# Kernel tuning notes

Hardware: AMD Instinct MI355X
Metric: run time of the kernel (lower is better)

## Reference

```python
import jax, jax.numpy as jnp
import numpy as np

B, L, C = 16, 450, 768
MID = 256
K = 8912
TEMP = 0.07
ENT_TEMP = 0.01
EPS_NORM = 1e-12


def _l2norm(v):
    n = jnp.sqrt(jnp.sum(v * v, axis=-1, keepdims=True))
    return v / jnp.maximum(n, EPS_NORM)


def setup_inputs() -> dict:
    key = jax.random.key(0)
    k1, k2, k3, k4 = jax.random.split(key, 4)
    x = jax.random.normal(k1, (B, L, C), dtype=jnp.float32)
    W_down = jax.random.normal(k2, (C, MID), dtype=jnp.float32) * (1.0 / np.sqrt(C))
    b_down = jnp.zeros((MID,), dtype=jnp.float32)
    bound = 1.0 / np.sqrt(MID)
    embedding = jax.random.uniform(k3, (K, MID), dtype=jnp.float32, minval=-bound, maxval=bound)
    return {"x": x, "W_down": W_down, "b_down": b_down, "embedding": embedding}


def reference(x, W_down, b_down, embedding):
    Bx, Lx, Cx = x.shape
    # down projection: [B,L,C] -> [B,L,MID]
    z = jnp.einsum('blc,cm->blm', x, W_down) + b_down
    zf = z.reshape(Bx * Lx, MID)
    zn = _l2norm(zf)                       # [N, MID]
    en = _l2norm(embedding)                # [K, MID]
    # squared euclidean distance on the unit sphere: ||a-b||^2 = 2 - 2 a.b
    d = 2.0 - 2.0 * jnp.einsum('nm,km->nk', zn, en)   # [N, K]
    idx = jnp.argmin(d, axis=1)            # [N]
    # codebook usage (no-grad stats)
    occ = jnp.bincount(idx, length=K)
    code_book_usage = jnp.mean((occ > 0).astype(jnp.float32))
    # soft assignment probs (hard_quant branch)
    logits = -d / TEMP
    probs = jax.nn.softmax(logits, axis=1)
    z_q = en[idx]                          # [N, MID]
    vq_loss = jnp.mean((z_q - jax.lax.stop_gradient(zn)) ** 2)
    commit_loss = jnp.mean((jax.lax.stop_gradient(z_q) - zn) ** 2)
    # straight-through estimator
    z_q_ste = zn + jax.lax.stop_gradient(z_q - zn)
    # entropy loss on affinity = -d at entropy temperature
    fa = -d / ENT_TEMP
    p = jax.nn.softmax(fa, axis=-1)
    lp = jax.nn.log_softmax(fa, axis=-1)
    avg_probs = jnp.mean(p, axis=0)
    avg_entropy = -jnp.sum(avg_probs * jnp.log(avg_probs + 1e-5))
    sample_entropy = -jnp.mean(jnp.sum(p * lp, axis=-1))
    entropy_loss = sample_entropy - avg_entropy
    return (z_q_ste.reshape(Bx, Lx, MID), probs.reshape(Bx, Lx, K),
            code_book_usage, vq_loss, commit_loss, entropy_loss)
```

## Files before the change

kernel.cpp:

```cpp
#include <hip/hip_runtime.h>
#include <stdint.h>

#define N_TOK 7200
#define N_PAD 7232
#define K_CODE 8912
#define K_PAD 8960
#define N_KT 140
#define MID 256
#define C_DIM 768
#define INV_TEMP (1.0f/0.07f)
#define INV_ETEMP 100.0f
#define MARGIN 0.02f
#define CAND_CAP 64
#define EPS_N 1e-12f

typedef __attribute__((ext_vector_type(8))) short short8;
typedef __attribute__((ext_vector_type(4))) float f32x4;

__device__ __forceinline__ unsigned short f2bf(float f) {
    unsigned u = __float_as_uint(f);
    u += 0x7fffu + ((u >> 16) & 1u);
    return (unsigned short)(u >> 16);
}
__device__ __forceinline__ float bf2f(unsigned short h) {
    return __uint_as_float(((unsigned)h) << 16);
}
__device__ __forceinline__ void nt_store4(float* p, float a, float b, float c, float d) {
    f32x4 v; v.x = a; v.y = b; v.z = c; v.w = d;
    __builtin_nontemporal_store(v, (f32x4*)p);
}

__global__ void k_prep(const float* __restrict__ emb,
                       float* __restrict__ en, unsigned short* __restrict__ en_h,
                       const float* __restrict__ W,
                       unsigned short* __restrict__ wt_h, unsigned short* __restrict__ wt_l,
                       const float* __restrict__ x,
                       unsigned short* __restrict__ xh_g, unsigned short* __restrict__ xl_g,
                       float* __restrict__ ap_acc, int* __restrict__ used,
                       float* __restrict__ acc4, int* __restrict__ ccnt) {
    __shared__ float sb[256];
    int b = blockIdx.x, t = threadIdx.x;
    if (b < K_CODE) {
        float v = emb[b * MID + t];
        sb[t] = v * v; __syncthreads();
        for (int s = 128; s > 0; s >>= 1) { if (t < s) sb[t] += sb[t + s]; __syncthreads(); }
        float nn = sqrtf(sb[0]);
        float o = v / fmaxf(nn, EPS_N);
        en[b * MID + t] = o;
        en_h[b * MID + t] = f2bf(o);
    } else if (b < K_CODE + 768) {
        int i = (b - K_CODE) * 256 + t;
        int c = i / MID, tc = i % MID;
        float v = W[i];
        unsigned short h = f2bf(v);
        unsigned short l = f2bf(v - bf2f(h));
        wt_h[tc * C_DIM + c] = h;
        wt_l[tc * C_DIM + c] = l;
    } else if (b < K_CODE + 768 + 5400) {
        size_t i4 = ((size_t)(b - K_CODE - 768) * 256 + t) * 4;
        float4 v = *(const float4*)(x + i4);
        unsigned short h0 = f2bf(v.x), h1 = f2bf(v.y), h2 = f2bf(v.z), h3 = f2bf(v.w);
        *((ushort4*)(xh_g + i4)) = make_ushort4(h0, h1, h2, h3);
        *((ushort4*)(xl_g + i4)) = make_ushort4(f2bf(v.x - bf2f(h0)), f2bf(v.y - bf2f(h1)),
                                                f2bf(v.z - bf2f(h2)), f2bf(v.w - bf2f(h3)));
    } else {
        int i = (b - K_CODE - 768 - 5400) * 256 + t;
        if (i < K_CODE) { ap_acc[i] = 0.f; used[i] = 0; }
        if (i < N_TOK) ccnt[i] = 0;
        if (i < 4) acc4[i] = 0.f;
    }
}

__global__ __launch_bounds__(256) void k_zgemm(const unsigned short* __restrict__ xh_g,
                                               const unsigned short* __restrict__ xl_g,
                                               const unsigned short* __restrict__ wt_h,
                                               const unsigned short* __restrict__ wt_l,
                                               float* __restrict__ zbuf) {
    __shared__ unsigned short ls[4 * 64 * 72];
    unsigned short* xh = ls;
    unsigned short* xl = ls + 64 * 72;
    unsigned short* wh = ls + 2 * 64 * 72;
    unsigned short* wl = ls + 3 * 64 * 72;
    int tid = threadIdx.x;
    int m0 = blockIdx.y * 64;
    int t0 = blockIdx.x * 64;
    int lane = tid & 63, wv = tid >> 6;
    int quad = lane >> 4, l15 = lane & 15;
    int mrow0 = (wv >> 1) * 32, ncol0 = (wv & 1) * 32;
    f32x4 acc[2][2] = {};

    for (int ch = 0; ch < 12; ch++) {
        int c0 = ch * 64;
        for (int it = 0; it < 2; it++) {
            int r = it * 32 + (tid >> 3);
            int cq = tid & 7;
            int gr = m0 + r;
            uint4 vh = make_uint4(0, 0, 0, 0), vl = make_uint4(0, 0, 0, 0);
            if (gr < N_TOK) {
                vh = ((const uint4*)xh_g)[(size_t)gr * (C_DIM / 8) + (c0 >> 3) + cq];
                vl = ((const uint4*)xl_g)[(size_t)gr * (C_DIM / 8) + (c0 >> 3) + cq];
            }
            *((uint4*)&xh[r * 72 + cq * 8]) = vh;
            *((uint4*)&xl[r * 72 + cq * 8]) = vl;
        }
        for (int it = 0; it < 2; it++) {
            int r = it * 32 + (tid >> 3);
            int cq = tid & 7;
            uint4 vh = ((const uint4*)wt_h)[(size_t)(t0 + r) * (C_DIM / 8) + (c0 >> 3) + cq];
            uint4 vl = ((const uint4*)wt_l)[(size_t)(t0 + r) * (C_DIM / 8) + (c0 >> 3) + cq];
            *((uint4*)&wh[r * 72 + cq * 8]) = vh;
            *((uint4*)&wl[r * 72 + cq * 8]) = vl;
        }
        __syncthreads();
        for (int ks = 0; ks < 2; ks++) {
            int co = ks * 32 + quad * 8;
            short8 ah0 = *((const short8*)&xh[(mrow0 + l15) * 72 + co]);
            short8 ah1 = *((const short8*)&xh[(mrow0 + 16 + l15) * 72 + co]);
            short8 al0 = *((const short8*)&xl[(mrow0 + l15) * 72 + co]);
            short8 al1 = *((const short8*)&xl[(mrow0 + 16 + l15) * 72 + co]);
            short8 bh0 = *((const short8*)&wh[(ncol0 + l15) * 72 + co]);
            short8 bh1 = *((const short8*)&wh[(ncol0 + 16 + l15) * 72 + co]);
            short8 bl0 = *((const short8*)&wl[(ncol0 + l15) * 72 + co]);
            short8 bl1 = *((const short8*)&wl[(ncol0 + 16 + l15) * 72 + co]);
            acc[0][0] = __builtin_amdgcn_mfma_f32_16x16x32_bf16(ah0, bh0, acc[0][0], 0, 0, 0);
            acc[0][1] = __builtin_amdgcn_mfma_f32_16x16x32_bf16(ah0, bh1, acc[0][1], 0, 0, 0);
            acc[1][0] = __builtin_amdgcn_mfma_f32_16x16x32_bf16(ah1, bh0, acc[1][0], 0, 0, 0);
            acc[1][1] = __builtin_amdgcn_mfma_f32_16x16x32_bf16(ah1, bh1, acc[1][1], 0, 0, 0);
            acc[0][0] = __builtin_amdgcn_mfma_f32_16x16x32_bf16(ah0, bl0, acc[0][0], 0, 0, 0);
            acc[0][1] = __builtin_amdgcn_mfma_f32_16x16x32_bf16(ah0, bl1, acc[0][1], 0, 0, 0);
            acc[1][0] = __builtin_amdgcn_mfma_f32_16x16x32_bf16(ah1, bl0, acc[1][0], 0, 0, 0);
            acc[1][1] = __builtin_amdgcn_mfma_f32_16x16x32_bf16(ah1, bl1, acc[1][1], 0, 0, 0);
            acc[0][0] = __builtin_amdgcn_mfma_f32_16x16x32_bf16(al0, bh0, acc[0][0], 0, 0, 0);
            acc[0][1] = __builtin_amdgcn_mfma_f32_16x16x32_bf16(al0, bh1, acc[0][1], 0, 0, 0);
            acc[1][0] = __builtin_amdgcn_mfma_f32_16x16x32_bf16(al1, bh0, acc[1][0], 0, 0, 0);
            acc[1][1] = __builtin_amdgcn_mfma_f32_16x16x32_bf16(al1, bh1, acc[1][1], 0, 0, 0);
        }
        __syncthreads();
    }
    for (int i = 0; i < 2; i++)
        for (int j = 0; j < 2; j++)
            for (int r = 0; r < 4; r++) {
                int gr = m0 + mrow0 + i * 16 + quad * 4 + r;
                int gc = t0 + ncol0 + j * 16 + l15;
                if (gr < N_TOK) zbuf[(size_t)gr * MID + gc] = acc[i][j][r];
            }
}

__global__ void k_znorm(float* __restrict__ zbuf, const float* __restrict__ b_down,
                        unsigned short* __restrict__ zn_h) {
    int n = blockIdx.x, t = threadIdx.x;
    float v = zbuf[(size_t)n * MID + t] + b_down[t];
    __shared__ float sb[256];
    sb[t] = v * v; __syncthreads();
    for (int s = 128; s > 0; s >>= 1) { if (t < s) sb[t] += sb[t + s]; __syncthreads(); }
    float nn = sqrtf(sb[0]);
    float o = v / fmaxf(nn, EPS_N);
    zbuf[(size_t)n * MID + t] = o;
    zn_h[(size_t)n * MID + t] = f2bf(o);
}

template<int PASS>
__global__ __launch_bounds__(256) void k_dpass(const unsigned short* __restrict__ zn_h,
                                               const unsigned short* __restrict__ en_h,
                                               float* __restrict__ part4,
                                               const float* __restrict__ rs_m,
                                               const float* __restrict__ rs_ist,
                                               const float* __restrict__ rs_is1,
                                               float* __restrict__ ap_acc,
                                               float* __restrict__ out1,
                                               int* __restrict__ ccnt,
                                               int* __restrict__ cand) {
    __shared__ __align__(16) char smem[32768];
    char* atB = smem;
    char* btB = smem + 16384;
    int tid = threadIdx.x;
    int kt = blockIdx.x, mt = blockIdx.y;
    int m0 = mt * 64, k0c = kt * 64;
    int lane = tid & 63, wv = tid >> 6;
    int quad = lane >> 4, l15 = lane & 15;
    int mrow0 = (wv >> 1) * 32, ncol0 = (wv & 1) * 32;
    f32x4 acc[2][2] = {};

    for (int ch = 0; ch < 2; ch++) {
        int c0 = ch * 128;
        for (int it = 0; it < 4; it++) {
            int r = it * 16 + (tid >> 4);
            int cq = tid & 15;
            uint4 va = ((const uint4*)zn_h)[(size_t)(m0 + r) * (MID / 8) + (c0 >> 3) + cq];
            uint4 vb = ((const uint4*)en_h)[(size_t)(k0c + r) * (MID / 8) + (c0 >> 3) + cq];
            int boff = r * 256 + ((cq * 16) ^ ((r & 7) << 4));
            *((uint4*)(atB + boff)) = va;
            *((uint4*)(btB + boff)) = vb;
        }
        __syncthreads();
        for (int ks = 0; ks < 4; ks++) {
            int co = ks * 64 + quad * 16;
            int ra0 = mrow0 + l15,      ra1 = mrow0 + 16 + l15;
            int rb0 = ncol0 + l15,      rb1 = ncol0 + 16 + l15;
            short8 a0 = *((const short8*)(atB + ra0 * 256 + (co ^ ((ra0 & 7) << 4))));
            short8 a1 = *((const short8*)(atB + ra1 * 256 + (co ^ ((ra1 & 7) << 4))));
            short8 b0 = *((const short8*)(btB + rb0 * 256 + (co ^ ((rb0 & 7) << 4))));
            short8 b1 = *((const short8*)(btB + rb1 * 256 + (co ^ ((rb1 & 7) << 4))));
            acc[0][0] = __builtin_amdgcn_mfma_f32_16x16x32_bf16(a0, b0, acc[0][0], 0, 0, 0);
            acc[0][1] = __builtin_amdgcn_mfma_f32_16x16x32_bf16(a0, b1, acc[0][1], 0, 0, 0);
            acc[1][0] = __builtin_amdgcn_mfma_f32_16x16x32_bf16(a1, b0, acc[1][0], 0, 0, 0);
            acc[1][1] = __builtin_amdgcn_mfma_f32_16x16x32_bf16(a1, b1, acc[1][1], 0, 0, 0);
        }
        __syncthreads();
    }

    float* sd = (float*)smem;
    float* lm = sd + 64 * 68;
    float* lt = lm + 64;
    float* l1 = lt + 64;
    float* colacc = l1 + 64;

    if (PASS == 2) {
        if (tid < 64) {
            int gr = m0 + tid;
            bool okr = gr < N_TOK;
            lm[tid] = okr ? rs_m[gr] : 0.f;
            lt[tid] = okr ? rs_ist[gr] : 0.f;
            l1[tid] = okr ? rs_is1[gr] : 0.f;
        }
    }
    for (int i = 0; i < 2; i++)
        for (int j = 0; j < 2; j++)
            for (int r = 0; r < 4; r++) {
                int lr = mrow0 + i * 16 + quad * 4 + r;
                int lc = ncol0 + j * 16 + l15;
                int gc = k0c + lc;
                float dv = (gc < K_CODE) ? (2.f - 2.f * acc[i][j][r]) : 1e30f;
                sd[lr * 68 + lc] = dv;
            }
    __syncthreads();

    if (PASS == 1) {
        int rloc = wv * 16 + (lane >> 2);
        const float* rowp = sd + rloc * 68 + (lane & 3) * 16;
        float vals[16];
        float vmin = 1e30f;
        #pragma unroll
        for (int i = 0; i < 16; i++) { vals[i] = rowp[i]; vmin = fminf(vmin, vals[i]); }
        vmin = fminf(vmin, __shfl_xor(vmin, 1));
        vmin = fminf(vmin, __shfl_xor(vmin, 2));
        float st = 0.f, s1 = 0.f, s2 = 0.f;
        #pragma unroll
        for (int i = 0; i < 16; i++) {
            float dd = vmin - vals[i];
            st += __expf(dd * INV_TEMP);
            float te = dd * INV_ETEMP;
            float e = __expf(te);
            s1 += e; s2 += e * te;
        }
        st += __shfl_xor(st, 1); st += __shfl_xor(st, 2);
        s1 += __shfl_xor(s1, 1); s1 += __shfl_xor(s1, 2);
        s2 += __shfl_xor(s2, 1); s2 += __shfl_xor(s2, 2);
        if ((lane & 3) == 0) {
            int gr = m0 + rloc;
            if (gr < N_TOK)
                nt_store4(part4 + ((size_t)gr * N_KT + kt) * 4, vmin, st, s1, s2);
        }
    } else {
        int col = tid & 63, rq = tid >> 6;
        float ce = 0.f;
        #pragma unroll
        for (int r16 = 0; r16 < 16; r16++) {
            int lr = rq * 16 + r16;
            float dv = sd[lr * 68 + col];
            ce += __expf((lm[lr] - dv) * INV_ETEMP) * l1[lr];
        }
        colacc[rq * 64 + col] = ce;
        __syncthreads();
        if (tid < 64) {
            float s = colacc[tid] + colacc[64 + tid] + colacc[128 + tid] + colacc[192 + tid];
            int gc = k0c + tid;
            if (gc < K_CODE) atomicAdd(&ap_acc[gc], s);
        }
        #pragma unroll
        for (int it = 0; it < 4; it++) {
            int idx = it * 256 + tid;
            int lr = idx >> 4, c4 = idx & 15;
            int gr = m0 + lr;
            if (gr >= N_TOK) continue;
            int gc = k0c + c4 * 4;
            if (gc >= K_CODE) continue;
            float4 v = *((const float4*)(sd + lr * 68 + c4 * 4));
            float mm = lm[lr], tt = lt[lr];
            float thr = mm + MARGIN;
            if (v.x <= thr) { int p = atomicAdd(&ccnt[gr], 1); if (p < CAND_CAP) cand[gr * CAND_CAP + p] = gc + 0; }
            if (v.y <= thr) { int p = atomicAdd(&ccnt[gr], 1); if (p < CAND_CAP) cand[gr * CAND_CAP + p] = gc + 1; }
            if (v.z <= thr) { int p = atomicAdd(&ccnt[gr], 1); if (p < CAND_CAP) cand[gr * CAND_CAP + p] = gc + 2; }
            if (v.w <= thr) { int p = atomicAdd(&ccnt[gr], 1); if (p < CAND_CAP) cand[gr * CAND_CAP + p] = gc + 3; }
            nt_store4(out1 + (size_t)gr * K_CODE + gc,
                      __expf((mm - v.x) * INV_TEMP) * tt,
                      __expf((mm - v.y) * INV_TEMP) * tt,
                      __expf((mm - v.z) * INV_TEMP) * tt,
                      __expf((mm - v.w) * INV_TEMP) * tt);
        }
    }
}

__global__ void k_combine(const float4* __restrict__ part4,
                          float* __restrict__ rs_m, float* __restrict__ rs_ist,
                          float* __restrict__ rs_is1,
                          float* __restrict__ acc4) {
    int sub = threadIdx.x >> 6;
    int row = blockIdx.x * 4 + sub;
    int l = threadIdx.x & 63;
    float4 pv[3];
    float m = 1e30f;
    #pragma unroll
    for (int c = 0; c < 3; c++) {
        int t = l + c * 64;
        pv[c] = (t < N_KT) ? part4[(size_t)row * N_KT + t] : make_float4(1e30f, 0.f, 0.f, 0.f);
        m = fminf(m, pv[c].x);
    }
    #pragma unroll
    for (int s = 1; s < 64; s <<= 1) m = fminf(m, __shfl_xor(m, s));
    float st = 0.f, s1 = 0.f, s2 = 0.f;
    #pragma unroll
    for (int c = 0; c < 3; c++) {
        float mb = pv[c].x;
        int t = l + c * 64;
        if (t < N_KT && mb < 1e29f) {
            float dT = (m - mb) * INV_TEMP;
            st += __expf(dT) * pv[c].y;
            float dE = (m - mb) * INV_ETEMP;
            float e = __expf(dE);
            s1 += e * pv[c].z;
            s2 += e * (pv[c].w + dE * pv[c].z);
        }
    }
    #pragma unroll
    for (int s = 1; s < 64; s <<= 1) {
        st += __shfl_xor(st, s);
        s1 += __shfl_xor(s1, s);
        s2 += __shfl_xor(s2, s);
    }
    if (l == 0) {
        rs_m[row] = m;
        rs_ist[row] = 1.f / st;
        rs_is1[row] = 1.f / s1;
        atomicAdd(&acc4[1], s2 / s1 - __logf(s1));
    }
}

__global__ void k_refine(const float* __restrict__ zn, const float* __restrict__ en,
                         const int* __restrict__ ccnt, const int* __restrict__ cand,
                         int* __restrict__ idxb, int* __restrict__ used,
                         float* __restrict__ acc4, float* __restrict__ out0) {
    int n = blockIdx.x * 4 + (threadIdx.x >> 6);
    int lane = threadIdx.x & 63;
    if (n >= N_TOK) return;
    int cnt = ccnt[n];
    if (cnt > CAND_CAP) cnt = CAND_CAP;
    float4 a = ((const float4*)(zn + (size_t)n * MID))[lane];
    float best = 1e30f; int bj = K_CODE;
    for (int c = 0; c < cnt; c++) {
        int code = cand[n * CAND_CAP + c];
        float4 b = ((const float4*)(en + (size_t)code * MID))[lane];
        float s = a.x * b.x + a.y * b.y + a.z * b.z + a.w * b.w;
        #pragma unroll
        for (int off = 1; off < 64; off <<= 1) s += __shfl_xor(s, off);
        float dist = 2.f - 2.f * s;
        if (dist < best || (dist == best && code < bj)) { best = dist; bj = code; }
    }
    float4 b = ((const float4*)(en + (size_t)bj * MID))[lane];
    nt_store4(out0 + (size_t)n * MID + lane * 4, b.x, b.y, b.z, b.w);
    float dx = b.x - a.x, dy = b.y - a.y, dz = b.z - a.z, dw = b.w - a.w;
    float sq = dx * dx + dy * dy + dz * dz + dw * dw;
    #pragma unroll
    for (int off = 32; off > 0; off >>= 1) sq += __shfl_down(sq, off);
    if (lane == 0) {
        idxb[n] = bj;
        used[bj] = 1;
        atomicAdd(&acc4[0], sq);
    }
}

__global__ void k_scal(const int* __restrict__ used, const float* __restrict__ ap_acc,
                       const float* __restrict__ acc4, float* __restrict__ outs) {
    int t = threadIdx.x;
    float uSum = 0.f, aeSum = 0.f;
    for (int k = t; k < K_CODE; k += 256) {
        uSum += (float)used[k];
        float ap = ap_acc[k] * (1.0f / (float)N_TOK);
        aeSum += ap * __logf(ap + 1e-5f);
    }
    __shared__ float sb[256];
    sb[t] = uSum; __syncthreads();
    for (int s = 128; s > 0; s >>= 1) { if (t < s) sb[t] += sb[t + s]; __syncthreads(); }
    uSum = sb[0];
    __syncthreads(); sb[t] = aeSum; __syncthreads();
    for (int s = 128; s > 0; s >>= 1) { if (t < s) sb[t] += sb[t + s]; __syncthreads(); }
    aeSum = sb[0];
    if (t == 0) {
        outs[0] = uSum / (float)K_CODE;
        float vq = acc4[0] / (float)((size_t)N_TOK * MID);
        outs[1] = vq;
        outs[2] = vq;
        outs[3] = -(acc4[1] / (float)N_TOK) + aeSum;
    }
}

extern "C" void kernel_launch(void* const* d_in, const int* in_sizes, int n_in,
                              void* d_out, int out_size, void* d_ws, size_t ws_size,
                              hipStream_t stream) {
    const float* x   = (const float*)d_in[0];
    const float* W   = (const float*)d_in[1];
    const float* b   = (const float*)d_in[2];
    const float* emb = (const float*)d_in[3];

    float* out  = (float*)d_out;
    float* out0 = out;
    float* out1 = out + (size_t)N_TOK * MID;
    float* outs = out + (size_t)N_TOK * MID + (size_t)N_TOK * K_CODE;

    char* w = (char*)d_ws;
    size_t off = 0;
    auto carve = [&](size_t bytes) { void* p = w + off; off += (bytes + 255) & ~(size_t)255; return p; };
    float*          zn    = (float*)         carve((size_t)N_PAD * MID * 4);
    float*          en    = (float*)         carve((size_t)K_PAD * MID * 4);
    unsigned short* zn_h  = (unsigned short*)carve((size_t)N_PAD * MID * 2);
    unsigned short* en_h  = (unsigned short*)carve((size_t)K_PAD * MID * 2);
    unsigned short* wt_h  = (unsigned short*)carve((size_t)MID * C_DIM * 2);
    unsigned short* wt_l  = (unsigned short*)carve((size_t)MID * C_DIM * 2);
    unsigned short* xh_g  = (unsigned short*)carve((size_t)N_TOK * C_DIM * 2);
    unsigned short* xl_g  = (unsigned short*)carve((size_t)N_TOK * C_DIM * 2);
    float*          part4 = (float*)         carve((size_t)N_TOK * N_KT * 16);
    float*          rs_m  = (float*)         carve((size_t)N_TOK * 4);
    float*          rs_ist= (float*)         carve((size_t)N_TOK * 4);
    float*          rs_is1= (float*)         carve((size_t)N_TOK * 4);
    int*            ccnt  = (int*)           carve((size_t)N_TOK * 4);
    int*            cand  = (int*)           carve((size_t)N_TOK * CAND_CAP * 4);
    int*            idxb  = (int*)           carve((size_t)N_TOK * 4);
    float*          ap_acc= (float*)         carve((size_t)K_CODE * 4);
    int*            used  = (int*)           carve((size_t)K_CODE * 4);
    float*          acc4  = (float*)         carve(16);
    (void)ws_size; (void)in_sizes; (void)n_in; (void)out_size;

    k_prep   <<<K_CODE + 768 + 5400 + 35, 256, 0, stream>>>(emb, en, en_h, W, wt_h, wt_l,
                                                            x, xh_g, xl_g,
                                                            ap_acc, used, acc4, ccnt);
    k_zgemm  <<<dim3(4, 113), 256, 0, stream>>>(xh_g, xl_g, wt_h, wt_l, zn);
    k_znorm  <<<N_TOK, 256, 0, stream>>>(zn, b, zn_h);
    k_dpass<1><<<dim3(N_KT, 113), 256, 0, stream>>>(zn_h, en_h, part4, rs_m, rs_ist, rs_is1, ap_acc, out1, ccnt, cand);
    k_combine<<<N_TOK / 4, 256, 0, stream>>>((const float4*)part4, rs_m, rs_ist, rs_is1, acc4);
    k_dpass<2><<<dim3(N_KT, 113), 256, 0, stream>>>(zn_h, en_h, part4, rs_m, rs_ist, rs_is1, ap_acc, out1, ccnt, cand);
    k_refine <<<N_TOK / 4, 256, 0, stream>>>(zn, en, ccnt, cand, idxb, used, acc4, out0);
    k_scal   <<<1, 256, 0, stream>>>(used, ap_acc, acc4, outs);
}
```

Baseline: 643.7 us.

## Replace second distance GEMM pass with rescale fixup over stored tile-local probabilities

The first pass now writes tile-local exp((tile_min - d)/TEMP) into the probs output. A new fixup kernel rescales each value by the global row max and normaliser, and derives candidate selection and the entropy column sums algebraically. Because ENT_TEMP/TEMP equals 7, the entropy term is obtained as a seventh power. This removes the recomputation of the full N×K GEMM in pass 2. In exchange the large probs buffer is read and written an extra time, and the powered values may lose precision or underflow.

```diff
diff --git a/kernel.cpp b/kernel.cpp
--- a/kernel.cpp
+++ b/kernel.cpp
@@ -159,17 +159,10 @@
     zn_h[(size_t)n * MID + t] = f2bf(o);
 }
 
-template<int PASS>
-__global__ __launch_bounds__(256) void k_dpass(const unsigned short* __restrict__ zn_h,
+__global__ __launch_bounds__(256) void k_dmain(const unsigned short* __restrict__ zn_h,
                                                const unsigned short* __restrict__ en_h,
                                                float* __restrict__ part4,
-                                               const float* __restrict__ rs_m,
-                                               const float* __restrict__ rs_ist,
-                                               const float* __restrict__ rs_is1,
-                                               float* __restrict__ ap_acc,
-                                               float* __restrict__ out1,
-                                               int* __restrict__ ccnt,
-                                               int* __restrict__ cand) {
+                                               float* __restrict__ out1) {
     __shared__ __align__(16) char smem[32768];
     char* atB = smem;
     char* btB = smem + 16384;
@@ -209,21 +202,9 @@
         __syncthreads();
     }
 
-    float* sd = (float*)smem;
-    float* lm = sd + 64 * 68;
-    float* lt = lm + 64;
-    float* l1 = lt + 64;
-    float* colacc = l1 + 64;
-
-    if (PASS == 2) {
-        if (tid < 64) {
-            int gr = m0 + tid;
-            bool okr = gr < N_TOK;
-            lm[tid] = okr ? rs_m[gr] : 0.f;
-            lt[tid] = okr ? rs_ist[gr] : 0.f;
-            l1[tid] = okr ? rs_is1[gr] : 0.f;
-        }
-    }
+    float* sd  = (float*)smem;
+    float* vmn = sd + 64 * 68;
+
     for (int i = 0; i < 2; i++)
         for (int j = 0; j < 2; j++)
             for (int r = 0; r < 4; r++) {
@@ -235,7 +216,7 @@
             }
     __syncthreads();
 
-    if (PASS == 1) {
+    {
         int rloc = wv * 16 + (lane >> 2);
         const float* rowp = sd + rloc * 68 + (lane & 3) * 16;
         float vals[16];
@@ -257,47 +238,30 @@
         s1 += __shfl_xor(s1, 1); s1 += __shfl_xor(s1, 2);
         s2 += __shfl_xor(s2, 1); s2 += __shfl_xor(s2, 2);
         if ((lane & 3) == 0) {
+            vmn[rloc] = vmin;
             int gr = m0 + rloc;
             if (gr < N_TOK)
                 nt_store4(part4 + ((size_t)gr * N_KT + kt) * 4, vmin, st, s1, s2);
         }
-    } else {
-        int col = tid & 63, rq = tid >> 6;
-        float ce = 0.f;
-        #pragma unroll
-        for (int r16 = 0; r16 < 16; r16++) {
-            int lr = rq * 16 + r16;
-            float dv = sd[lr * 68 + col];
-            ce += __expf((lm[lr] - dv) * INV_ETEMP) * l1[lr];
-        }
-        colacc[rq * 64 + col] = ce;
-        __syncthreads();
-        if (tid < 64) {
-            float s = colacc[tid] + colacc[64 + tid] + colacc[128 + tid] + colacc[192 + tid];
-            int gc = k0c + tid;
-            if (gc < K_CODE) atomicAdd(&ap_acc[gc], s);
-        }
-        #pragma unroll
-        for (int it = 0; it < 4; it++) {
-            int idx = it * 256 + tid;
-            int lr = idx >> 4, c4 = idx & 15;
-            int gr = m0 + lr;
-            if (gr >= N_TOK) continue;
-            int gc = k0c + c4 * 4;
-            if (gc >= K_CODE) continue;
-            float4 v = *((const float4*)(sd + lr * 68 + c4 * 4));
-            float mm = lm[lr], tt = lt[lr];
-            float thr = mm + MARGIN;
-            if (v.x <= thr) { int p = atomicAdd(&ccnt[gr], 1); if (p < CAND_CAP) cand[gr * CAND_CAP + p] = gc + 0; }
-            if (v.y <= thr) { int p = atomicAdd(&ccnt[gr], 1); if (p < CAND_CAP) cand[gr * CAND_CAP + p] = gc + 1; }
-            if (v.z <= thr) { int p = atomicAdd(&ccnt[gr], 1); if (p < CAND_CAP) cand[gr * CAND_CAP + p] = gc + 2; }
-            if (v.w <= thr) { int p = atomicAdd(&ccnt[gr], 1); if (p < CAND_CAP) cand[gr * CAND_CAP + p] = gc + 3; }
-            nt_store4(out1 + (size_t)gr * K_CODE + gc,
-                      __expf((mm - v.x) * INV_TEMP) * tt,
-                      __expf((mm - v.y) * INV_TEMP) * tt,
-                      __expf((mm - v.z) * INV_TEMP) * tt,
-                      __expf((mm - v.w) * INV_TEMP) * tt);
-        }
+    }
+    __syncthreads();
+
+    #pragma unroll
+    for (int it = 0; it < 4; it++) {
+        int idx = it * 256 + tid;
+        int lr = idx >> 4, c4 = idx & 15;
+        int gr = m0 + lr;
+        if (gr >= N_TOK) continue;
+        int gc = k0c + c4 * 4;
+        if (gc >= K_CODE) continue;
+        float4 v = *((const float4*)(sd + lr * 68 + c4 * 4));
+        float vm = vmn[lr];
+        float4 p;
+        p.x = __expf((vm - v.x) * INV_TEMP);
+        p.y = __expf((vm - v.y) * INV_TEMP);
+        p.z = __expf((vm - v.z) * INV_TEMP);
+        p.w = __expf((vm - v.w) * INV_TEMP);
+        *((float4*)(out1 + (size_t)gr * K_CODE + gc)) = p;
     }
 }
 
@@ -343,6 +307,72 @@
         rs_ist[row] = 1.f / st;
         rs_is1[row] = 1.f / s1;
         atomicAdd(&acc4[1], s2 / s1 - __logf(s1));
+    }
+}
+
+__global__ __launch_bounds__(256) void k_fix(float* __restrict__ out1,
+                                             const float* __restrict__ part4,
+                                             const float* __restrict__ rs_m,
+                                             const float* __restrict__ rs_ist,
+                                             const float* __restrict__ rs_is1,
+                                             float* __restrict__ ap_acc,
+                                             int* __restrict__ ccnt,
+                                             int* __restrict__ cand) {
+    __shared__ float sS[128 * 4], sT[128 * 4], sE[128 * 4];
+    __shared__ float colacc[4 * 256];
+    int ct = blockIdx.x, rt = blockIdx.y;
+    int r0 = rt * 128, c0 = ct * 256;
+    int t = threadIdx.x;
+    for (int p = t; p < 512; p += 256) {
+        int row = p >> 2, k4 = p & 3;
+        int gr = r0 + row;
+        float s = 0.f, th = 1e30f, e = 0.f;
+        if (gr < N_TOK) {
+            int kt = (c0 >> 6) + k4;
+            float vmin = part4[((size_t)gr * N_KT + kt) * 4];
+            float m = rs_m[gr];
+            s  = __expf((m - vmin) * INV_TEMP) * rs_ist[gr];
+            th = __expf((vmin - m - MARGIN) * INV_TEMP);
+            e  = __expf((m - vmin) * INV_ETEMP) * rs_is1[gr];
+        }
+        sS[p] = s; sT[p] = th; sE[p] = e;
+    }
+    __syncthreads();
+    int g = t >> 6;
+    int colq = (t & 63) * 4;
+    int k4 = colq >> 6;
+    int gc = c0 + colq;
+    float ce0 = 0.f, ce1 = 0.f, ce2 = 0.f, ce3 = 0.f;
+    if (gc < K_CODE) {
+        for (int i = 0; i < 32; i++) {
+            int lr = g * 32 + i;
+            int gr = r0 + lr;
+            if (gr >= N_TOK) break;
+            size_t base = (size_t)gr * K_CODE + gc;
+            float4 pt = *(const float4*)(out1 + base);
+            int idx = lr * 4 + k4;
+            float s = sS[idx], th = sT[idx], e = sE[idx];
+            nt_store4(out1 + base, pt.x * s, pt.y * s, pt.z * s, pt.w * s);
+            if (pt.x >= th) { int p = atomicAdd(&ccnt[gr], 1); if (p < CAND_CAP) cand[gr * CAND_CAP + p] = gc + 0; }
+            if (pt.y >= th) { int p = atomicAdd(&ccnt[gr], 1); if (p < CAND_CAP) cand[gr * CAND_CAP + p] = gc + 1; }
+            if (pt.z >= th) { int p = atomicAdd(&ccnt[gr], 1); if (p < CAND_CAP) cand[gr * CAND_CAP + p] = gc + 2; }
+            if (pt.w >= th) { int p = atomicAdd(&ccnt[gr], 1); if (p < CAND_CAP) cand[gr * CAND_CAP + p] = gc + 3; }
+            float a, a2, a4;
+            a = pt.x; a2 = a * a; a4 = a2 * a2; ce0 += a4 * a2 * a * e;
+            a = pt.y; a2 = a * a; a4 = a2 * a2; ce1 += a4 * a2 * a * e;
+            a = pt.z; a2 = a * a; a4 = a2 * a2; ce2 += a4 * a2 * a * e;
+            a = pt.w; a2 = a * a; a4 = a2 * a2; ce3 += a4 * a2 * a * e;
+        }
+    }
+    colacc[g * 256 + colq + 0] = ce0;
+    colacc[g * 256 + colq + 1] = ce1;
+    colacc[g * 256 + colq + 2] = ce2;
+    colacc[g * 256 + colq + 3] = ce3;
+    __syncthreads();
+    {
+        float ssum = colacc[t] + colacc[256 + t] + colacc[512 + t] + colacc[768 + t];
+        int c = c0 + t;
+        if (c < K_CODE) atomicAdd(&ap_acc[c], ssum);
     }
 }
 
@@ -445,9 +475,9 @@
                                                             ap_acc, used, acc4, ccnt);
     k_zgemm  <<<dim3(4, 113), 256, 0, stream>>>(xh_g, xl_g, wt_h, wt_l, zn);
     k_znorm  <<<N_TOK, 256, 0, stream>>>(zn, b, zn_h);
-    k_dpass<1><<<dim3(N_KT, 113), 256, 0, stream>>>(zn_h, en_h, part4, rs_m, rs_ist, rs_is1, ap_acc, out1, ccnt, cand);
+    k_dmain  <<<dim3(N_KT, 113), 256, 0, stream>>>(zn_h, en_h, part4, out1);
     k_combine<<<N_TOK / 4, 256, 0, stream>>>((const float4*)part4, rs_m, rs_ist, rs_is1, acc4);
-    k_dpass<2><<<dim3(N_KT, 113), 256, 0, stream>>>(zn_h, en_h, part4, rs_m, rs_ist, rs_is1, ap_acc, out1, ccnt, cand);
+    k_fix    <<<dim3(35, 57), 256, 0, stream>>>(out1, part4, rs_m, rs_ist, rs_is1, ap_acc, ccnt, cand);
     k_refine <<<N_TOK / 4, 256, 0, stream>>>(zn, en, ccnt, cand, idxb, used, acc4, out0);
     k_scal   <<<1, 256, 0, stream>>>(used, ap_acc, acc4, outs);
 }
```

Measured after the change: 679.6 us. 5.6% more time.
